# Performance work log

Measured on AMD Instinct MI355X. Metric: run time of the kernel, lower is better.

Reference implementation:

```python
import jax, jax.numpy as jnp
import numpy as np
import math

B, S, D = 2, 2048, 1024
H = 16
HD = D // H
W = 128


def setup_inputs() -> dict:
    key = jax.random.key(0)
    ks = jax.random.split(key, 5)
    scale = 1.0 / math.sqrt(D)
    return {
        "x": jax.random.normal(ks[0], (B, S, D), dtype=jnp.float32),
        "in_proj_w": jax.random.normal(ks[1], (3 * D, D), dtype=jnp.float32) * scale,
        "in_proj_b": jax.random.normal(ks[2], (3 * D,), dtype=jnp.float32) * 0.02,
        "out_proj_w": jax.random.normal(ks[3], (D, D), dtype=jnp.float32) * scale,
        "out_proj_b": jax.random.normal(ks[4], (D,), dtype=jnp.float32) * 0.02,
        "window_size": W,
    }


def reference(x, in_proj_w, in_proj_b, out_proj_w, out_proj_b, window_size):
    b, s, d = x.shape
    # Combined qkv projection, as nn.MultiheadAttention does
    qkv = x @ in_proj_w.T + in_proj_b  # [B,S,3D]
    q, k, v = jnp.split(qkv, 3, axis=-1)
    # [B,H,S,HD]
    def heads(t):
        return t.reshape(b, s, H, HD).transpose(0, 2, 1, 3)
    q, k, v = heads(q), heads(k), heads(v)
    scale = 1.0 / math.sqrt(HD)
    scores = jnp.einsum("bhqd,bhkd->bhqk", q, k) * scale  # [B,H,S,S]
    # banded sliding-window mask: disallow |i-j| > window_size
    i = jnp.arange(s)[:, None]
    j = jnp.arange(s)[None, :]
    banned = jnp.abs(i - j) > window_size  # [S,S] bool
    scores = jnp.where(banned[None, None], -jnp.inf, scores)
    attn = jax.nn.softmax(scores, axis=-1)
    out = jnp.einsum("bhqk,bhkd->bhqd", attn, v)  # [B,H,S,HD]
    out = out.transpose(0, 2, 1, 3).reshape(b, s, d)
    return out @ out_proj_w.T + out_proj_b
```

## Files before the change

kernel.cpp:

```cpp
#include <hip/hip_runtime.h>

#define S_LEN 2048
#define DMODEL 1024
#define NHEAD 16
#define HDIM 64

typedef __bf16 bf16x8 __attribute__((ext_vector_type(8)));
typedef float f32x4 __attribute__((ext_vector_type(4)));

typedef __attribute__((address_space(1))) const void gconst_void;
typedef __attribute__((address_space(3))) void lds_void;

__device__ __forceinline__ unsigned short f2bf(float f) {
    unsigned u = __builtin_bit_cast(unsigned, f);
    u += 0x7fffu + ((u >> 16) & 1u);
    return (unsigned short)(u >> 16);
}

#define N4_X  (2 * S_LEN * DMODEL / 4)
#define N4_W1 (3 * DMODEL * DMODEL / 4)
#define N4_W2 (DMODEL * DMODEL / 4)
__global__ __launch_bounds__(256) void cvt_all(const float* __restrict__ x,
                                               const float* __restrict__ w1,
                                               const float* __restrict__ w2,
                                               unsigned short* __restrict__ xb,
                                               unsigned short* __restrict__ w1b,
                                               unsigned short* __restrict__ w2b) {
    int i = blockIdx.x * 256 + threadIdx.x;
    const float* s;
    unsigned short* d;
    int off;
    if (i < N4_X)            { s = x;  d = xb;  off = i; }
    else if (i < N4_X + N4_W1) { s = w1; d = w1b; off = i - N4_X; }
    else if (i < N4_X + N4_W1 + N4_W2) { s = w2; d = w2b; off = i - N4_X - N4_W1; }
    else return;
    float4 f = ((const float4*)s)[off];
    ushort4 o;
    o.x = f2bf(f.x); o.y = f2bf(f.y); o.z = f2bf(f.z); o.w = f2bf(f.w);
    ((ushort4*)d)[off] = o;
}

__global__ __launch_bounds__(256) void gemm_qkv(const unsigned short* __restrict__ A,
                                                const unsigned short* __restrict__ Bt,
                                                const float* __restrict__ bias,
                                                unsigned short* __restrict__ qk,
                                                unsigned short* __restrict__ vT,
                                                int M, int N, int K) {
    __shared__ unsigned short lds[128 * 64 * 2] __attribute__((aligned(16)));
    unsigned short* lA = lds;
    unsigned short* lB = lds + 128 * 64;

    const int tid  = threadIdx.x;
    const int lane = tid & 63;
    const int w    = tid >> 6;
    const int quad = lane >> 4;
    const int l16  = lane & 15;

    const int m0 = blockIdx.x * 128;
    const int n0 = blockIdx.y * 128;

    const int rowi = tid >> 3;
    const int csw  = ((tid & 7) ^ (rowi & 7)) * 8;
    const unsigned short* aSrc = A + (size_t)(m0 + rowi) * K + csw;
    const unsigned short* bSrc = Bt + (size_t)(n0 + rowi) * K + csw;
    const int dstOff = (w * 8) * 64;

    f32x4 acc[4][4];
    {
        f32x4 z = {0.f, 0.f, 0.f, 0.f};
        #pragma unroll
        for (int i = 0; i < 4; i++)
            #pragma unroll
            for (int j = 0; j < 4; j++) acc[i][j] = z;
    }

    const int wm = (w & 1) * 64;
    const int wn = (w >> 1) * 64;

    for (int kt = 0; kt < K; kt += 64) {
        __syncthreads();
        #pragma unroll
        for (int p = 0; p < 4; p++) {
            __builtin_amdgcn_global_load_lds(
                (gconst_void*)(aSrc + (size_t)p * 32 * K + kt),
                (lds_void*)(&lA[dstOff + p * 32 * 64]), 16, 0, 0);
            __builtin_amdgcn_global_load_lds(
                (gconst_void*)(bSrc + (size_t)p * 32 * K + kt),
                (lds_void*)(&lB[dstOff + p * 32 * 64]), 16, 0, 0);
        }
        __syncthreads();

        #pragma unroll
        for (int kk = 0; kk < 2; kk++) {
            bf16x8 af[4], bfr[4];
            const int xsw = ((kk * 4 + quad) ^ (l16 & 7)) * 8;
            #pragma unroll
            for (int t = 0; t < 4; t++) {
                af[t]  = *(const bf16x8*)&lA[(wm + t * 16 + l16) * 64 + xsw];
                bfr[t] = *(const bf16x8*)&lB[(wn + t * 16 + l16) * 64 + xsw];
            }
            #pragma unroll
            for (int i = 0; i < 4; i++)
                #pragma unroll
                for (int j = 0; j < 4; j++)
                    acc[i][j] = __builtin_amdgcn_mfma_f32_16x16x32_bf16(af[i], bfr[j], acc[i][j], 0, 0, 0);
        }
    }

    if (n0 < 2 * DMODEL) {
        #pragma unroll
        for (int j = 0; j < 4; j++) {
            const int n = n0 + wn + j * 16 + l16;
            const float bv = bias[n];
            const float scl = (n < DMODEL) ? 0.125f : 1.0f;
            #pragma unroll
            for (int i = 0; i < 4; i++) {
                const int mrow = m0 + wm + i * 16 + quad * 4;
                #pragma unroll
                for (int r = 0; r < 4; r++) {
                    float v = (acc[i][j][r] + bv) * scl;
                    qk[(size_t)(mrow + r) * 2048 + n] = f2bf(v);
                }
            }
        }
    } else {
        __syncthreads();
        unsigned short* T = lds;
        #pragma unroll
        for (int j = 0; j < 4; j++) {
            const int nl = wn + j * 16 + l16;
            const float bv = bias[n0 + nl];
            #pragma unroll
            for (int i = 0; i < 4; i++) {
                const int ml0 = wm + i * 16 + quad * 4;
                ushort4 pk;
                pk.x = f2bf(acc[i][j][0] + bv);
                pk.y = f2bf(acc[i][j][1] + bv);
                pk.z = f2bf(acc[i][j][2] + bv);
                pk.w = f2bf(acc[i][j][3] + bv);
                const int addr = nl * 128 + (((ml0 >> 3) ^ (nl & 7)) << 3) + (ml0 & 7);
                *(ushort4*)&T[addr] = pk;
            }
        }
        __syncthreads();
        const int b  = m0 >> 11;
        const int sg = m0 & (S_LEN - 1);
        const int hd0 = n0 - 2 * DMODEL;
        const int sc = (tid & 15) << 3;
        #pragma unroll
        for (int pass = 0; pass < 8; pass++) {
            const int dl = (tid >> 4) + pass * 16;
            bf16x8 val = *(const bf16x8*)&T[dl * 128 + ((((sc >> 3) ^ (dl & 7)) & 15) << 3)];
            *(bf16x8*)&vT[(size_t)(b * DMODEL + hd0 + dl) * S_LEN + sg + sc] = val;
        }
    }
}

__global__ __launch_bounds__(256) void gemm_out(const unsigned short* __restrict__ A,
                                                const unsigned short* __restrict__ Bt,
                                                const float* __restrict__ bias,
                                                float* __restrict__ out,
                                                int M, int N, int K) {
    __shared__ unsigned short lA[128 * 64] __attribute__((aligned(16)));
    __shared__ unsigned short lB[64 * 64] __attribute__((aligned(16)));

    const int tid  = threadIdx.x;
    const int lane = tid & 63;
    const int w    = tid >> 6;
    const int quad = lane >> 4;
    const int l16  = lane & 15;

    const int m0 = blockIdx.x * 128;
    const int n0 = blockIdx.y * 64;

    const int rowi = tid >> 3;
    const int csw  = ((tid & 7) ^ (rowi & 7)) * 8;
    const unsigned short* aSrc = A + (size_t)(m0 + rowi) * K + csw;
    const unsigned short* bSrc = Bt + (size_t)(n0 + rowi) * K + csw;
    const int dstOff = (w * 8) * 64;

    f32x4 acc[4][2];
    {
        f32x4 z = {0.f, 0.f, 0.f, 0.f};
        #pragma unroll
        for (int i = 0; i < 4; i++) { acc[i][0] = z; acc[i][1] = z; }
    }

    const int wm = (w & 1) * 64;
    const int wn = (w >> 1) * 32;

    for (int kt = 0; kt < K; kt += 64) {
        __syncthreads();
        #pragma unroll
        for (int p = 0; p < 4; p++) {
            __builtin_amdgcn_global_load_lds(
                (gconst_void*)(aSrc + (size_t)p * 32 * K + kt),
                (lds_void*)(&lA[dstOff + p * 32 * 64]), 16, 0, 0);
        }
        #pragma unroll
        for (int p = 0; p < 2; p++) {
            __builtin_amdgcn_global_load_lds(
                (gconst_void*)(bSrc + (size_t)p * 32 * K + kt),
                (lds_void*)(&lB[dstOff + p * 32 * 64]), 16, 0, 0);
        }
        __syncthreads();

        #pragma unroll
        for (int kk = 0; kk < 2; kk++) {
            bf16x8 af[4], bfr[2];
            const int xsw = ((kk * 4 + quad) ^ (l16 & 7)) * 8;
            #pragma unroll
            for (int t = 0; t < 4; t++)
                af[t] = *(const bf16x8*)&lA[(wm + t * 16 + l16) * 64 + xsw];
            #pragma unroll
            for (int t = 0; t < 2; t++)
                bfr[t] = *(const bf16x8*)&lB[(wn + t * 16 + l16) * 64 + xsw];
            #pragma unroll
            for (int i = 0; i < 4; i++)
                #pragma unroll
                for (int j = 0; j < 2; j++)
                    acc[i][j] = __builtin_amdgcn_mfma_f32_16x16x32_bf16(af[i], bfr[j], acc[i][j], 0, 0, 0);
        }
    }

    #pragma unroll
    for (int j = 0; j < 2; j++) {
        const int n = n0 + wn + j * 16 + l16;
        const float bv = bias[n];
        #pragma unroll
        for (int i = 0; i < 4; i++) {
            const int mrow = m0 + wm + i * 16 + quad * 4;
            #pragma unroll
            for (int r = 0; r < 4; r++)
                out[(size_t)(mrow + r) * N + n] = acc[i][j][r] + bv;
        }
    }
}

__global__ __launch_bounds__(256) void attn_win(const unsigned short* __restrict__ qk,
                                                const unsigned short* __restrict__ vT,
                                                unsigned short* __restrict__ attnout,
                                                const int* __restrict__ wptr) {
    __shared__ unsigned short lP[4][16 * 32] __attribute__((aligned(16)));

    const int W = wptr[0];
    const int tid  = threadIdx.x;
    const int lane = tid & 63;
    const int w    = tid >> 6;
    const int quad = lane >> 4;
    const int l16  = lane & 15;

    const int q0 = blockIdx.x * 64;
    const int h  = blockIdx.y;
    const size_t rowbase = (size_t)blockIdx.z * S_LEN;

    const int qrow = q0 + w * 16 + l16;
    bf16x8 qf0, qf1;
    {
        const unsigned short* qp = qk + (rowbase + qrow) * (2 * DMODEL) + h * HDIM;
        qf0 = *(const bf16x8*)(qp + quad * 8);
        qf1 = *(const bf16x8*)(qp + 32 + quad * 8);
    }

    const unsigned short* kbasep = qk + rowbase * (2 * DMODEL) + DMODEL + h * HDIM;
    const unsigned short* vbase  = vT + (size_t)(blockIdx.z * DMODEL + h * HDIM) * S_LEN;

    f32x4 o[4];
    { f32x4 z = {0.f,0.f,0.f,0.f}; o[0]=z; o[1]=z; o[2]=z; o[3]=z; }
    float lsum[4] = {0.f, 0.f, 0.f, 0.f};

    const int kbase = q0 - W;
    const int nch = (2 * W + 64 + 31) / 32;
    const int iq = q0 + w * 16 + quad * 4;

    for (int c = 0; c < nch; c++) {
        const int kc0 = kbase + c * 32;

        int kr0 = kc0 + l16;       kr0 = kr0 < 0 ? 0 : (kr0 > S_LEN - 1 ? S_LEN - 1 : kr0);
        int kr1 = kc0 + 16 + l16;  kr1 = kr1 < 0 ? 0 : (kr1 > S_LEN - 1 ? S_LEN - 1 : kr1);
        const unsigned short* kp0 = kbasep + (size_t)kr0 * (2 * DMODEL) + quad * 8;
        const unsigned short* kp1 = kbasep + (size_t)kr1 * (2 * DMODEL) + quad * 8;
        bf16x8 k0lo = *(const bf16x8*)(kp0);
        bf16x8 k0hi = *(const bf16x8*)(kp0 + 32);
        bf16x8 k1lo = *(const bf16x8*)(kp1);
        bf16x8 k1hi = *(const bf16x8*)(kp1 + 32);

        f32x4 s0 = {0.f,0.f,0.f,0.f}, s1 = {0.f,0.f,0.f,0.f};
        s0 = __builtin_amdgcn_mfma_f32_16x16x32_bf16(qf0, k0lo, s0, 0, 0, 0);
        s0 = __builtin_amdgcn_mfma_f32_16x16x32_bf16(qf1, k0hi, s0, 0, 0, 0);
        s1 = __builtin_amdgcn_mfma_f32_16x16x32_bf16(qf0, k1lo, s1, 0, 0, 0);
        s1 = __builtin_amdgcn_mfma_f32_16x16x32_bf16(qf1, k1hi, s1, 0, 0, 0);

        const int j0 = kc0 + l16;
        const int j1 = j0 + 16;
        #pragma unroll
        for (int r = 0; r < 4; r++) {
            const int i = iq + r;
            const int d0 = i - j0, d1 = i - j1;
            const bool v0 = ((unsigned)j0 < (unsigned)S_LEN) && (d0 <= W) && (-d0 <= W);
            const bool v1 = ((unsigned)j1 < (unsigned)S_LEN) && (d1 <= W) && (-d1 <= W);
            float p0 = v0 ? __expf(s0[r]) : 0.f;
            float p1 = v1 ? __expf(s1[r]) : 0.f;
            lsum[r] += p0 + p1;
            const int qq = quad * 4 + r;
            const int sw = (qq >> 1) & 3;
            lP[w][qq * 32 + (((l16 >> 3) ^ sw) & 3) * 8 + (l16 & 7)] = f2bf(p0);
            lP[w][qq * 32 + ((((l16 >> 3) + 2) ^ sw) & 3) * 8 + (l16 & 7)] = f2bf(p1);
        }

        __builtin_amdgcn_s_waitcnt(0xc07f);

        bf16x8 pf = *(const bf16x8*)&lP[w][l16 * 32 + ((quad ^ ((l16 >> 1) & 3)) & 3) * 8];
        int sc = kc0 + quad * 8;
        sc = sc < 0 ? 0 : (sc > S_LEN - 8 ? S_LEN - 8 : sc);
        #pragma unroll
        for (int t = 0; t < 4; t++) {
            bf16x8 vf = *(const bf16x8*)(vbase + (size_t)(t * 16 + l16) * S_LEN + sc);
            o[t] = __builtin_amdgcn_mfma_f32_16x16x32_bf16(pf, vf, o[t], 0, 0, 0);
        }
    }

    #pragma unroll
    for (int r = 0; r < 4; r++) {
        float l = lsum[r];
        l += __shfl_xor(l, 1);
        l += __shfl_xor(l, 2);
        l += __shfl_xor(l, 4);
        l += __shfl_xor(l, 8);
        const float inv = 1.f / l;
        #pragma unroll
        for (int t = 0; t < 4; t++) {
            attnout[(rowbase + iq + r) * DMODEL + h * HDIM + t * 16 + l16] = f2bf(o[t][r] * inv);
        }
    }
}

extern "C" void kernel_launch(void* const* d_in, const int* in_sizes, int n_in,
                              void* d_out, int out_size, void* d_ws, size_t ws_size,
                              hipStream_t stream) {
    const float* x   = (const float*)d_in[0];
    const float* w1  = (const float*)d_in[1];
    const float* b1  = (const float*)d_in[2];
    const float* w2  = (const float*)d_in[3];
    const float* b2  = (const float*)d_in[4];
    const int* wsz   = (const int*)d_in[5];

    char* ws = (char*)d_ws;
    unsigned short* xb    = (unsigned short*)(ws);
    unsigned short* attnb = (unsigned short*)(ws);
    unsigned short* w1b   = (unsigned short*)(ws + (8u << 20));
    unsigned short* w2b   = (unsigned short*)(ws + (14u << 20));
    unsigned short* qkb   = (unsigned short*)(ws + (16u << 20));
    unsigned short* vTb   = (unsigned short*)(ws + (32u << 20));

    const int M = 2 * S_LEN;

    cvt_all<<<(N4_X + N4_W1 + N4_W2 + 255) / 256, 256, 0, stream>>>(x, w1, w2, xb, w1b, w2b);

    gemm_qkv<<<dim3(M / 128, 3 * DMODEL / 128), 256, 0, stream>>>(xb, w1b, b1, qkb, vTb, M, 3 * DMODEL, DMODEL);

    attn_win<<<dim3(S_LEN / 64, NHEAD, 2), 256, 0, stream>>>(qkb, vTb, attnb, wsz);

    gemm_out<<<dim3(M / 128, DMODEL / 64), 256, 0, stream>>>(attnb, w2b, b2, (float*)d_out, M, DMODEL, DMODEL);
}
```

Measured before the change: 187.9 us.

## Stage K/V tiles in LDS for window attention and widen out-proj GEMM tile

The attention kernel now loads 64-key K and V chunks cooperatively into LDS with async global-to-LDS copies, shared by all four waves. Before, each wave fetched K and V directly from global memory per 32-key chunk. It also computes scores for 64 keys per chunk and skips per-element masking when a chunk lies entirely inside the window. The output projection GEMM grows its N tile from 64 to 128, so each wave holds a 4x4 accumulator grid. The aim is to improve data reuse and MFMA density, at the cost of more registers, added block barriers, and half as many blocks for the output GEMM.

Result: faster. 171.5 us (-8.7%).

```diff
diff --git a/kernel.cpp b/kernel.cpp
--- a/kernel.cpp
+++ b/kernel.cpp
@@ -162,7 +162,7 @@
                                                 float* __restrict__ out,
                                                 int M, int N, int K) {
     __shared__ unsigned short lA[128 * 64] __attribute__((aligned(16)));
-    __shared__ unsigned short lB[64 * 64] __attribute__((aligned(16)));
+    __shared__ unsigned short lB[128 * 64] __attribute__((aligned(16)));
 
     const int tid  = threadIdx.x;
     const int lane = tid & 63;
@@ -171,7 +171,7 @@
     const int l16  = lane & 15;
 
     const int m0 = blockIdx.x * 128;
-    const int n0 = blockIdx.y * 64;
+    const int n0 = blockIdx.y * 128;
 
     const int rowi = tid >> 3;
     const int csw  = ((tid & 7) ^ (rowi & 7)) * 8;
@@ -179,15 +179,17 @@
     const unsigned short* bSrc = Bt + (size_t)(n0 + rowi) * K + csw;
     const int dstOff = (w * 8) * 64;
 
-    f32x4 acc[4][2];
+    f32x4 acc[4][4];
     {
         f32x4 z = {0.f, 0.f, 0.f, 0.f};
         #pragma unroll
-        for (int i = 0; i < 4; i++) { acc[i][0] = z; acc[i][1] = z; }
+        for (int i = 0; i < 4; i++)
+            #pragma unroll
+            for (int j = 0; j < 4; j++) acc[i][j] = z;
     }
 
     const int wm = (w & 1) * 64;
-    const int wn = (w >> 1) * 32;
+    const int wn = (w >> 1) * 64;
 
     for (int kt = 0; kt < K; kt += 64) {
         __syncthreads();
@@ -196,9 +198,6 @@
             __builtin_amdgcn_global_load_lds(
                 (gconst_void*)(aSrc + (size_t)p * 32 * K + kt),
                 (lds_void*)(&lA[dstOff + p * 32 * 64]), 16, 0, 0);
-        }
-        #pragma unroll
-        for (int p = 0; p < 2; p++) {
             __builtin_amdgcn_global_load_lds(
                 (gconst_void*)(bSrc + (size_t)p * 32 * K + kt),
                 (lds_void*)(&lB[dstOff + p * 32 * 64]), 16, 0, 0);
@@ -207,24 +206,23 @@
 
         #pragma unroll
         for (int kk = 0; kk < 2; kk++) {
-            bf16x8 af[4], bfr[2];
+            bf16x8 af[4], bfr[4];
             const int xsw = ((kk * 4 + quad) ^ (l16 & 7)) * 8;
             #pragma unroll
-            for (int t = 0; t < 4; t++)
-                af[t] = *(const bf16x8*)&lA[(wm + t * 16 + l16) * 64 + xsw];
-            #pragma unroll
-            for (int t = 0; t < 2; t++)
+            for (int t = 0; t < 4; t++) {
+                af[t]  = *(const bf16x8*)&lA[(wm + t * 16 + l16) * 64 + xsw];
                 bfr[t] = *(const bf16x8*)&lB[(wn + t * 16 + l16) * 64 + xsw];
+            }
             #pragma unroll
             for (int i = 0; i < 4; i++)
                 #pragma unroll
-                for (int j = 0; j < 2; j++)
+                for (int j = 0; j < 4; j++)
                     acc[i][j] = __builtin_amdgcn_mfma_f32_16x16x32_bf16(af[i], bfr[j], acc[i][j], 0, 0, 0);
         }
     }
 
     #pragma unroll
-    for (int j = 0; j < 2; j++) {
+    for (int j = 0; j < 4; j++) {
         const int n = n0 + wn + j * 16 + l16;
         const float bv = bias[n];
         #pragma unroll
@@ -241,7 +239,9 @@
                                                 const unsigned short* __restrict__ vT,
                                                 unsigned short* __restrict__ attnout,
                                                 const int* __restrict__ wptr) {
-    __shared__ unsigned short lP[4][16 * 32] __attribute__((aligned(16)));
+    __shared__ unsigned short lK[64 * 64] __attribute__((aligned(16)));
+    __shared__ unsigned short lV[64 * 64] __attribute__((aligned(16)));
+    __shared__ unsigned short lP[4][16 * 64] __attribute__((aligned(16)));
 
     const int W = wptr[0];
     const int tid  = threadIdx.x;
@@ -269,54 +269,95 @@
     { f32x4 z = {0.f,0.f,0.f,0.f}; o[0]=z; o[1]=z; o[2]=z; o[3]=z; }
     float lsum[4] = {0.f, 0.f, 0.f, 0.f};
 
+    const int iq = q0 + w * 16 + quad * 4;
+    int lo[4], hi[4];
+    #pragma unroll
+    for (int r = 0; r < 4; r++) {
+        const int i = iq + r;
+        lo[r] = max(i - W, 0);
+        hi[r] = min(i + W, S_LEN - 1);
+    }
+
     const int kbase = q0 - W;
-    const int nch = (2 * W + 64 + 31) / 32;
-    const int iq = q0 + w * 16 + quad * 4;
+    const int nch = (2 * W + 64 + 63) >> 6;
+
+    const int skey = tid >> 3;
+    const int sch  = tid & 7;
+    const unsigned short* ldsKdst = &lK[(size_t)w * 512];
+    const unsigned short* ldsVdst = &lV[(size_t)w * 512];
 
     for (int c = 0; c < nch; c++) {
-        const int kc0 = kbase + c * 32;
-
-        int kr0 = kc0 + l16;       kr0 = kr0 < 0 ? 0 : (kr0 > S_LEN - 1 ? S_LEN - 1 : kr0);
-        int kr1 = kc0 + 16 + l16;  kr1 = kr1 < 0 ? 0 : (kr1 > S_LEN - 1 ? S_LEN - 1 : kr1);
-        const unsigned short* kp0 = kbasep + (size_t)kr0 * (2 * DMODEL) + quad * 8;
-        const unsigned short* kp1 = kbasep + (size_t)kr1 * (2 * DMODEL) + quad * 8;
-        bf16x8 k0lo = *(const bf16x8*)(kp0);
-        bf16x8 k0hi = *(const bf16x8*)(kp0 + 32);
-        bf16x8 k1lo = *(const bf16x8*)(kp1);
-        bf16x8 k1hi = *(const bf16x8*)(kp1 + 32);
-
-        f32x4 s0 = {0.f,0.f,0.f,0.f}, s1 = {0.f,0.f,0.f,0.f};
-        s0 = __builtin_amdgcn_mfma_f32_16x16x32_bf16(qf0, k0lo, s0, 0, 0, 0);
-        s0 = __builtin_amdgcn_mfma_f32_16x16x32_bf16(qf1, k0hi, s0, 0, 0, 0);
-        s1 = __builtin_amdgcn_mfma_f32_16x16x32_bf16(qf0, k1lo, s1, 0, 0, 0);
-        s1 = __builtin_amdgcn_mfma_f32_16x16x32_bf16(qf1, k1hi, s1, 0, 0, 0);
-
-        const int j0 = kc0 + l16;
-        const int j1 = j0 + 16;
+        const int kc0 = kbase + c * 64;
+        if (kc0 >= S_LEN || kc0 + 63 < 0) continue;
+
+        __syncthreads();
+        #pragma unroll
+        for (int p = 0; p < 2; p++) {
+            const int row = p * 32 + skey;
+            const int cs  = sch ^ (row & 7);
+            int kg = kc0 + row;
+            kg = kg < 0 ? 0 : (kg > S_LEN - 1 ? S_LEN - 1 : kg);
+            __builtin_amdgcn_global_load_lds(
+                (gconst_void*)(kbasep + (size_t)kg * (2 * DMODEL) + cs * 8),
+                (lds_void*)(ldsKdst + p * 2048), 16, 0, 0);
+            int s0a = kc0 + cs * 8;
+            s0a = s0a < 0 ? 0 : (s0a > S_LEN - 8 ? S_LEN - 8 : s0a);
+            __builtin_amdgcn_global_load_lds(
+                (gconst_void*)(vbase + (size_t)row * S_LEN + s0a),
+                (lds_void*)(ldsVdst + p * 2048), 16, 0, 0);
+        }
+        __syncthreads();
+
+        f32x4 s4[4];
+        { f32x4 z = {0.f,0.f,0.f,0.f}; s4[0]=z; s4[1]=z; s4[2]=z; s4[3]=z; }
+        #pragma unroll
+        for (int half = 0; half < 2; half++) {
+            const bf16x8 qf = half ? qf1 : qf0;
+            const int cs = half * 4 + quad;
+            #pragma unroll
+            for (int kt = 0; kt < 4; kt++) {
+                const int key = kt * 16 + l16;
+                bf16x8 kf = *(const bf16x8*)&lK[key * 64 + ((cs ^ (key & 7)) << 3)];
+                s4[kt] = __builtin_amdgcn_mfma_f32_16x16x32_bf16(qf, kf, s4[kt], 0, 0, 0);
+            }
+        }
+
+        const bool fullvalid = (kc0 >= 0) && (kc0 + 63 < S_LEN) &&
+                               (kc0 >= q0 + 63 - W) && (kc0 + 63 <= q0 + W);
         #pragma unroll
         for (int r = 0; r < 4; r++) {
-            const int i = iq + r;
-            const int d0 = i - j0, d1 = i - j1;
-            const bool v0 = ((unsigned)j0 < (unsigned)S_LEN) && (d0 <= W) && (-d0 <= W);
-            const bool v1 = ((unsigned)j1 < (unsigned)S_LEN) && (d1 <= W) && (-d1 <= W);
-            float p0 = v0 ? __expf(s0[r]) : 0.f;
-            float p1 = v1 ? __expf(s1[r]) : 0.f;
-            lsum[r] += p0 + p1;
-            const int qq = quad * 4 + r;
-            const int sw = (qq >> 1) & 3;
-            lP[w][qq * 32 + (((l16 >> 3) ^ sw) & 3) * 8 + (l16 & 7)] = f2bf(p0);
-            lP[w][qq * 32 + ((((l16 >> 3) + 2) ^ sw) & 3) * 8 + (l16 & 7)] = f2bf(p1);
+            const int q = quad * 4 + r;
+            const int qsw = q & 7;
+            float ps = 0.f;
+            #pragma unroll
+            for (int kt = 0; kt < 4; kt++) {
+                float p;
+                if (fullvalid) {
+                    p = __expf(s4[kt][r]);
+                } else {
+                    const int j = kc0 + kt * 16 + l16;
+                    const bool v = (j >= lo[r]) && (j <= hi[r]);
+                    p = v ? __expf(s4[kt][r]) : 0.f;
+                }
+                ps += p;
+                const int ct = kt * 2 + (l16 >> 3);
+                lP[w][q * 64 + ((ct ^ qsw) << 3) + (l16 & 7)] = f2bf(p);
+            }
+            lsum[r] += ps;
         }
 
         __builtin_amdgcn_s_waitcnt(0xc07f);
 
-        bf16x8 pf = *(const bf16x8*)&lP[w][l16 * 32 + ((quad ^ ((l16 >> 1) & 3)) & 3) * 8];
-        int sc = kc0 + quad * 8;
-        sc = sc < 0 ? 0 : (sc > S_LEN - 8 ? S_LEN - 8 : sc);
-        #pragma unroll
-        for (int t = 0; t < 4; t++) {
-            bf16x8 vf = *(const bf16x8*)(vbase + (size_t)(t * 16 + l16) * S_LEN + sc);
-            o[t] = __builtin_amdgcn_mfma_f32_16x16x32_bf16(pf, vf, o[t], 0, 0, 0);
+        #pragma unroll
+        for (int ks = 0; ks < 2; ks++) {
+            const int cs = ks * 4 + quad;
+            bf16x8 pf = *(const bf16x8*)&lP[w][l16 * 64 + ((cs ^ (l16 & 7)) << 3)];
+            #pragma unroll
+            for (int dt = 0; dt < 4; dt++) {
+                const int d = dt * 16 + l16;
+                bf16x8 vf = *(const bf16x8*)&lV[d * 64 + ((cs ^ (d & 7)) << 3)];
+                o[dt] = __builtin_amdgcn_mfma_f32_16x16x32_bf16(pf, vf, o[dt], 0, 0, 0);
+            }
         }
     }
 
@@ -361,5 +402,5 @@
 
     attn_win<<<dim3(S_LEN / 64, NHEAD, 2), 256, 0, stream>>>(qkb, vTb, attnb, wsz);
 
-    gemm_out<<<dim3(M / 128, DMODEL / 64), 256, 0, stream>>>(attnb, w2b, b2, (float*)d_out, M, DMODEL, DMODEL);
-}
+    gemm_out<<<dim3(M / 128, DMODEL / 128), 256, 0, stream>>>(attnb, w2b, b2, (float*)d_out, M, DMODEL, DMODEL);
+}
```
